# Kernel optimization log

Hardware: AMD Instinct MI355X
Metric: run time of the kernel (lower is better)

The kernel has to match this reference:

```python
import jax, jax.numpy as jnp
import numpy as np

SR = 16000
HOP = 256
MIN_F0 = 50.0
MAX_F0 = 500.0
MIN_PERIOD = SR // 500          # 32
MAX_PERIOD = SR // 50           # 320
FRAME_LEN = HOP * 2             # 512
LAG_END = min(MAX_PERIOD, FRAME_LEN // 2)  # 256 -> lags 32..255 (224 lags)


def setup_inputs() -> dict:
    key = jax.random.key(0)
    waveform = jax.random.normal(key, (64, 1, 163840), dtype=jnp.float32)
    return {"waveform": waveform}


def reference(waveform):
    B, C, T = waveform.shape
    x = waveform[:, 0, :]  # (B, T)
    pad = FRAME_LEN // 2
    xpad = jnp.pad(x, ((0, 0), (pad, pad)), mode='reflect')
    n_frames = (T + 2 * pad - FRAME_LEN) // HOP + 1  # = T//HOP + 1
    # frame extraction (equivalent to unfold(frame_length, hop))
    idx = np.arange(n_frames)[:, None] * HOP + np.arange(FRAME_LEN)[None, :]
    frames = xpad[:, idx]  # (B, F, L)
    # L2-normalize each frame
    norm = jnp.sqrt(jnp.sum(frames * frames, axis=-1, keepdims=True))
    xn = frames / (norm + 1e-8)
    # zero-pad right so xn[t] * xz[t+p] reproduces frame[:L-p] * frame[p:]
    xz = jnp.pad(xn, ((0, 0), (0, 0), (0, FRAME_LEN)))
    lags = jnp.arange(MIN_PERIOD, LAG_END)

    def step(carry, p):
        sl = jax.lax.dynamic_slice_in_dim(xz, p, FRAME_LEN, axis=-1)
        return carry, jnp.sum(xn * sl, axis=-1)  # (B, F)

    _, ac = jax.lax.scan(step, None, lags)  # (P, B, F)
    max_idx = jnp.argmax(ac, axis=0)  # (B, F)
    period = max_idx.astype(jnp.float32) + MIN_PERIOD
    f0 = SR / (period + 1e-8)
    return jnp.clip(f0, MIN_F0, MAX_F0)  # (B, F)
```

## Files before the change

### kernel.cpp

```cpp
#include <hip/hip_runtime.h>


#define SR_F 16000.0f
#define HOP 256
#define FRAME_LEN 512
#define PAD 256
#define T_LEN 163840
#define N_FRAMES 641
#define MIN_PERIOD 32
#define N_LAGS 224
#define WPB 4

typedef _Float16 half8 __attribute__((ext_vector_type(8)));
typedef float floatx4 __attribute__((ext_vector_type(4)));

__device__ __forceinline__ int swz(int q) { return q ^ ((q >> 3) & 7); }

__device__ __forceinline__ unsigned int pkh(float a, float b) {
    unsigned short ha = __builtin_bit_cast(unsigned short, (_Float16)a);
    unsigned short hb = __builtin_bit_cast(unsigned short, (_Float16)b);
    return (unsigned int)ha | ((unsigned int)hb << 16);
}

__device__ __forceinline__ void write_copies(unsigned int* e, unsigned int* o,
                                             unsigned int u10, unsigned int u11,
                                             unsigned int u20, unsigned int u21,
                                             int lane) {
    e[120 + 2*lane] = u10;  e[121 + 2*lane] = u11;
    e[248 + 2*lane] = u20;  e[249 + 2*lane] = u21;
    unsigned int a  = __shfl(u10, (lane + 1) & 63);
    unsigned int bb = __shfl(u20, (lane + 1) & 63);
    unsigned int n1 = (lane == 63) ? bb : a;
    unsigned int n2 = (lane == 63) ? 0u : bb;
    o[120 + 2*lane] = (u10 >> 16) | (u11 << 16);
    o[121 + 2*lane] = (u11 >> 16) | (n1 << 16);
    o[248 + 2*lane] = (u20 >> 16) | (u21 << 16);
    o[249 + 2*lane] = (u21 >> 16) | (n2 << 16);
    if (lane == 0) o[119] = u10 << 16;
}

__global__ __launch_bounds__(256, 4) void f0_kernel(const float* __restrict__ wav,
                                                    float* __restrict__ out) {
    __shared__ unsigned int yw[WPB][1600];

    const int tid  = threadIdx.x;
    const int wv   = tid >> 6;
    const int lane = tid & 63;
    unsigned int* ye  = yw[wv];
    unsigned int* yo  = ye + 400;
    unsigned int* le  = ye + 800;
    unsigned int* loo = ye + 1200;

    const int xcd = blockIdx.x & 7;
    const int idx = blockIdx.x >> 3;
    const int bf  = (xcd * 1282 + idx) * WPB + wv;
    const int b   = bf / N_FRAMES;
    const int f   = bf - b * N_FRAMES;
    const float* __restrict__ x = wav + (size_t)b * T_LEN;
    const int base = f * HOP - PAD;
    const bool fast = (f != 0 && f != N_FRAMES - 1);

    const int qd = lane >> 4;
    const int nn = lane & 15;
    const int par = nn & 1;
    const unsigned int* ybh = par ? yo : ye;
    const unsigned int* ybl = par ? loo : le;
    const int wA0 = 120 + 4*qd - 8*nn;
    const int wB0 = 136 + 4*qd + ((nn - par) >> 1);
    const int seg = lane & 15;
    const bool s0 = (seg & 1), s1 = (seg & 2), s2 = (seg & 4), s3 = (seg & 8);

    float4 c1, c2;
    if (fast) {
        const float4* g4 = (const float4*)(x + base);
        c1 = g4[lane];
        c2 = g4[lane + 64];
    }
    ye[lane] = 0u; yo[lane] = 0u;
    if (lane < 56) { ye[64 + lane] = 0u; yo[64 + lane] = 0u; }
    if (lane < 25) { ye[375 + lane] = 0u; yo[375 + lane] = 0u; }

    float qen = 0.0f;
    if (fast) {
        qen = c1.x*c1.x + c1.y*c1.y + c1.z*c1.z + c1.w*c1.w
            + c2.x*c2.x + c2.y*c2.y + c2.z*c2.z + c2.w*c2.w;
        write_copies(ye, yo, pkh(c1.x, c1.y), pkh(c1.z, c1.w),
                             pkh(c2.x, c2.y), pkh(c2.z, c2.w), lane);
    } else {
        for (int t = lane; t < FRAME_LEN; t += 64) {
            int idxr = base + t;
            if (idxr < 0) idxr = -idxr;
            if (idxr >= T_LEN) idxr = 2 * (T_LEN - 1) - idxr;
            float v = x[idxr];
            qen = __builtin_fmaf(v, v, qen);
            unsigned short h = __builtin_bit_cast(unsigned short, (_Float16)v);
            ((unsigned short*)ye)[240 + t] = h;
            ((unsigned short*)yo)[239 + t] = h;
        }
    }
    __threadfence_block();

    #pragma unroll
    for (int m = 1; m < 64; m <<= 1) qen += __shfl_xor(qen, m);

    floatx4 acc0 = {0.f, 0.f, 0.f, 0.f};
    floatx4 acc1 = {0.f, 0.f, 0.f, 0.f};
    #pragma unroll
    for (int c = 0; c < 16; c += 2) {
        uint4 au0 = *(const uint4*)(ye + (wA0 + 16*c));
        const unsigned int* pb0 = ybh + (wB0 + 16*c);
        uint4 bu0; bu0.x=pb0[0]; bu0.y=pb0[1]; bu0.z=pb0[2]; bu0.w=pb0[3];
        uint4 au1 = *(const uint4*)(ye + (wA0 + 16*(c+1)));
        const unsigned int* pb1 = ybh + (wB0 + 16*(c+1));
        uint4 bu1; bu1.x=pb1[0]; bu1.y=pb1[1]; bu1.z=pb1[2]; bu1.w=pb1[3];
        acc0 = __builtin_amdgcn_mfma_f32_16x16x32_f16(
            __builtin_bit_cast(half8, au0), __builtin_bit_cast(half8, bu0),
            acc0, 0, 0, 0);
        acc1 = __builtin_amdgcn_mfma_f32_16x16x32_f16(
            __builtin_bit_cast(half8, au1), __builtin_bit_cast(half8, bu1),
            acc1, 0, 0, 0);
    }
    floatx4 acc = acc0 + acc1;

    float v1 = acc[0];
    int   i1 = 64*qd + nn;
    float v2 = -__builtin_inff();
    #pragma unroll
    for (int r = 1; r < 4; ++r) {
        float cv = (4*qd + r < 14) ? acc[r] : -__builtin_inff();
        bool take = (cv > v1);
        float lose = take ? v1 : cv;
        if (take) { v1 = cv; i1 = 64*qd + 16*r + nn; }
        v2 = fmaxf(v2, lose);
    }
    #pragma unroll
    for (int m = 1; m < 64; m <<= 1) {
        float ov1 = __shfl_xor(v1, m);
        float ov2 = __shfl_xor(v2, m);
        int   oi1 = __shfl_xor(i1, m);
        bool take = (ov1 > v1) || (ov1 == v1 && oi1 < i1);
        float lose = take ? v1 : ov1;
        if (take) { v1 = ov1; i1 = oi1; }
        v2 = fmaxf(fmaxf(v2, ov2), lose);
    }

    const float E1 = 9.765625e-4f * qen + 0.05f;
    if (v1 - v2 > 2.0f * E1) {
        if (lane == 0) {
            float period = (float)(i1 + MIN_PERIOD);
            float f0 = SR_F / (period + 1e-8f);
            out[bf] = fminf(fmaxf(f0, 50.0f), 500.0f);
        }
        return;
    }

    le[lane] = 0u; loo[lane] = 0u;
    if (lane < 56) { le[64 + lane] = 0u; loo[64 + lane] = 0u; }
    if (lane < 25) { le[375 + lane] = 0u; loo[375 + lane] = 0u; }
    if (fast) {
        float l0 = c1.x - (float)(_Float16)c1.x;
        float l1 = c1.y - (float)(_Float16)c1.y;
        float l2 = c1.z - (float)(_Float16)c1.z;
        float l3 = c1.w - (float)(_Float16)c1.w;
        float l4 = c2.x - (float)(_Float16)c2.x;
        float l5 = c2.y - (float)(_Float16)c2.y;
        float l6 = c2.z - (float)(_Float16)c2.z;
        float l7 = c2.w - (float)(_Float16)c2.w;
        write_copies(le, loo, pkh(l0, l1), pkh(l2, l3),
                              pkh(l4, l5), pkh(l6, l7), lane);
    } else {
        for (int t = lane; t < FRAME_LEN; t += 64) {
            int idxr = base + t;
            if (idxr < 0) idxr = -idxr;
            if (idxr >= T_LEN) idxr = 2 * (T_LEN - 1) - idxr;
            float v = x[idxr];
            float l = v - (float)(_Float16)v;
            unsigned short h = __builtin_bit_cast(unsigned short, (_Float16)l);
            ((unsigned short*)le)[240 + t] = h;
            ((unsigned short*)loo)[239 + t] = h;
        }
    }
    __threadfence_block();

    #pragma unroll
    for (int c = 0; c < 16; ++c) {
        uint4 au = *(const uint4*)(ye + (wA0 + 16*c));
        const unsigned int* pb = ybl + (wB0 + 16*c);
        uint4 bu; bu.x = pb[0]; bu.y = pb[1]; bu.z = pb[2]; bu.w = pb[3];
        acc = __builtin_amdgcn_mfma_f32_16x16x32_f16(
            __builtin_bit_cast(half8, au), __builtin_bit_cast(half8, bu),
            acc, 0, 0, 0);
    }
    #pragma unroll
    for (int c = 0; c < 16; ++c) {
        uint4 au = *(const uint4*)(le + (wA0 + 16*c));
        const unsigned int* pb = ybh + (wB0 + 16*c);
        uint4 bu; bu.x = pb[0]; bu.y = pb[1]; bu.z = pb[2]; bu.w = pb[3];
        acc = __builtin_amdgcn_mfma_f32_16x16x32_f16(
            __builtin_bit_cast(half8, au), __builtin_bit_cast(half8, bu),
            acc, 0, 0, 0);
    }

    v1 = acc[0]; i1 = 64*qd + nn; v2 = -__builtin_inff();
    #pragma unroll
    for (int r = 1; r < 4; ++r) {
        float cv = (4*qd + r < 14) ? acc[r] : -__builtin_inff();
        bool take = (cv > v1);
        float lose = take ? v1 : cv;
        if (take) { v1 = cv; i1 = 64*qd + 16*r + nn; }
        v2 = fmaxf(v2, lose);
    }
    #pragma unroll
    for (int m = 1; m < 64; m <<= 1) {
        float ov1 = __shfl_xor(v1, m);
        float ov2 = __shfl_xor(v2, m);
        int   oi1 = __shfl_xor(i1, m);
        bool take = (ov1 > v1) || (ov1 == v1 && oi1 < i1);
        float lose = take ? v1 : ov1;
        if (take) { v1 = ov1; i1 = oi1; }
        v2 = fmaxf(fmaxf(v2, ov2), lose);
    }

    const float E2 = 1.0e-4f * qen + 0.02f;
    if (v1 - v2 > 2.0f * E2) {
        if (lane == 0) {
            float period = (float)(i1 + MIN_PERIOD);
            float f0 = SR_F / (period + 1e-8f);
            out[bf] = fminf(fmaxf(f0, 50.0f), 500.0f);
        }
        return;
    }

    float* sw = (float*)ye;
    if (fast) {
        const float4* g4 = (const float4*)(x + base);
        ((float4*)sw)[swz(lane)]      = g4[lane];
        ((float4*)sw)[swz(lane + 64)] = g4[lane + 64];
        if (lane < 16) ((float4*)sw)[swz(lane + 128)] = make_float4(0.f,0.f,0.f,0.f);
    } else {
        for (int t = lane; t < FRAME_LEN; t += 64) {
            int idxr = base + t;
            if (idxr < 0) idxr = -idxr;
            if (idxr >= T_LEN) idxr = 2 * (T_LEN - 1) - idxr;
            sw[(swz(t >> 2) << 2) | (t & 3)] = x[idxr];
        }
        int t = FRAME_LEN + lane;
        sw[(swz(t >> 2) << 2) | (t & 3)] = 0.0f;
    }
    __threadfence_block();

    const float4* s4 = (const float4*)sw;
    double dtot[4];
    #pragma unroll
    for (int r = 0; r < 4; ++r) {
        const int g  = (r << 2) + qd;
        const int p0 = MIN_PERIOD + (g << 4);
        double dacc[16];
        #pragma unroll
        for (int j = 0; j < 16; ++j) dacc[j] = 0.0;
        if (g < 14) {
            const int n16 = (FRAME_LEN - p0 + 15) >> 4;
            #pragma unroll
            for (int k = 0; k < 2; ++k) {
                const int ch = seg + (k << 4);
                if (ch < n16) {
                    const int t  = ch << 4;
                    const int qa = t >> 2;
                    const int qw = (t + p0) >> 2;
                    float a[16], w[32];
                    #pragma unroll
                    for (int u = 0; u < 4; ++u) {
                        float4 v = s4[swz(qa + u)];
                        a[4*u+0]=v.x; a[4*u+1]=v.y; a[4*u+2]=v.z; a[4*u+3]=v.w;
                    }
                    #pragma unroll
                    for (int u = 0; u < 8; ++u) {
                        float4 v = s4[swz(qw + u)];
                        w[4*u+0]=v.x; w[4*u+1]=v.y; w[4*u+2]=v.z; w[4*u+3]=v.w;
                    }
                    #pragma unroll
                    for (int j = 0; j < 16; ++j) {
                        #pragma unroll
                        for (int i = 0; i < 16; ++i)
                            dacc[j] = fma((double)a[i], (double)w[i + j], dacc[j]);
                    }
                }
            }
        }
        double u8[8], u4[4], u2[2], dtotal;
        #pragma unroll
        for (int i = 0; i < 8; ++i) {
            double lo = dacc[2*i], hi = dacc[2*i+1];
            double keep = s0 ? hi : lo, send = s0 ? lo : hi;
            u8[i] = keep + __shfl_xor(send, 1);
        }
        #pragma unroll
        for (int i = 0; i < 4; ++i) {
            double lo = u8[2*i], hi = u8[2*i+1];
            double keep = s1 ? hi : lo, send = s1 ? lo : hi;
            u4[i] = keep + __shfl_xor(send, 2);
        }
        #pragma unroll
        for (int i = 0; i < 2; ++i) {
            double lo = u4[2*i], hi = u4[2*i+1];
            double keep = s2 ? hi : lo, send = s2 ? lo : hi;
            u2[i] = keep + __shfl_xor(send, 4);
        }
        {
            double lo = u2[0], hi = u2[1];
            double keep = s3 ? hi : lo, send = s3 ? lo : hi;
            dtotal = keep + __shfl_xor(send, 8);
        }
        dtot[r] = ((r << 6) + lane < N_LAGS) ? dtotal : -__builtin_inf();
    }
    double dv1 = dtot[0];
    int    di1 = lane;
    #pragma unroll
    for (int r = 1; r < 4; ++r) {
        double c = dtot[r];
        if (c > dv1) { dv1 = c; di1 = (r << 6) + lane; }
    }
    #pragma unroll
    for (int m = 1; m < 64; m <<= 1) {
        double o = __shfl_xor(dv1, m);
        int   oi = __shfl_xor(di1, m);
        if (o > dv1 || (o == dv1 && oi < di1)) { dv1 = o; di1 = oi; }
    }
    if (lane == 0) {
        float period = (float)(di1 + MIN_PERIOD);
        float f0 = SR_F / (period + 1e-8f);
        out[bf] = fminf(fmaxf(f0, 50.0f), 500.0f);
    }
}

extern "C" void kernel_launch(void* const* d_in, const int* in_sizes, int n_in,
                              void* d_out, int out_size, void* d_ws, size_t ws_size,
                              hipStream_t stream) {
    const float* wav = (const float*)d_in[0];
    float* out = (float*)d_out;
    const int n_blocks = (64 * N_FRAMES) / WPB;
    f0_kernel<<<n_blocks, 256, 0, stream>>>(wav, out);
}
```

Baseline: 133.1 us.

## Split tiered f0 refinement into separate kernels with compacted work lists

Replaces the single kernel, in which each wave could fall through up to three precision tiers, with three kernels. A cheap fp16 MFMA pass handles every frame and appends ambiguous frames to a global list via atomics. A second kernel does the hi/lo split-precision pass only on the listed frames, and a third does the fp64 exact pass on what remains. Each kernel gets its own LDS footprint and launch bounds, so the common tier runs at higher occupancy and the rare tiers are not stranded in divergent waves. This adds extra launches, global atomics and list traffic, and the later kernels are sized with fixed grids whatever the list length.

```diff
diff --git a/kernel.cpp b/kernel.cpp
--- a/kernel.cpp
+++ b/kernel.cpp
@@ -7,12 +7,30 @@
 #define PAD 256
 #define T_LEN 163840
 #define N_FRAMES 641
+#define TOTAL (64 * N_FRAMES)
 #define MIN_PERIOD 32
 #define N_LAGS 224
-#define WPB 4
+
+#define A_BLOCKS 1536
+#define A_WPB 4
+#define A_WAVES (A_BLOCKS * A_WPB)
+#define A_CHUNK 7
+
+#define B_BLOCKS 512
+#define B_WPB 4
+#define B_WAVES (B_BLOCKS * B_WPB)
+
+#define C_BLOCKS 128
+#define C_WPB 4
+#define C_WAVES (C_BLOCKS * C_WPB)
 
 typedef _Float16 half8 __attribute__((ext_vector_type(8)));
 typedef float floatx4 __attribute__((ext_vector_type(4)));
+
+__device__ unsigned int g_cnt2;
+__device__ unsigned int g_cnt3;
+__device__ unsigned int g_lst2[TOTAL];
+__device__ unsigned int g_lst3[TOTAL];
 
 __device__ __forceinline__ int swz(int q) { return q ^ ((q >> 3) & 7); }
 
@@ -39,70 +57,9 @@
     if (lane == 0) o[119] = u10 << 16;
 }
 
-__global__ __launch_bounds__(256, 4) void f0_kernel(const float* __restrict__ wav,
-                                                    float* __restrict__ out) {
-    __shared__ unsigned int yw[WPB][1600];
-
-    const int tid  = threadIdx.x;
-    const int wv   = tid >> 6;
-    const int lane = tid & 63;
-    unsigned int* ye  = yw[wv];
-    unsigned int* yo  = ye + 400;
-    unsigned int* le  = ye + 800;
-    unsigned int* loo = ye + 1200;
-
-    const int xcd = blockIdx.x & 7;
-    const int idx = blockIdx.x >> 3;
-    const int bf  = (xcd * 1282 + idx) * WPB + wv;
-    const int b   = bf / N_FRAMES;
-    const int f   = bf - b * N_FRAMES;
-    const float* __restrict__ x = wav + (size_t)b * T_LEN;
-    const int base = f * HOP - PAD;
-    const bool fast = (f != 0 && f != N_FRAMES - 1);
-
-    const int qd = lane >> 4;
-    const int nn = lane & 15;
-    const int par = nn & 1;
-    const unsigned int* ybh = par ? yo : ye;
-    const unsigned int* ybl = par ? loo : le;
-    const int wA0 = 120 + 4*qd - 8*nn;
-    const int wB0 = 136 + 4*qd + ((nn - par) >> 1);
-    const int seg = lane & 15;
-    const bool s0 = (seg & 1), s1 = (seg & 2), s2 = (seg & 4), s3 = (seg & 8);
-
-    float4 c1, c2;
-    if (fast) {
-        const float4* g4 = (const float4*)(x + base);
-        c1 = g4[lane];
-        c2 = g4[lane + 64];
-    }
-    ye[lane] = 0u; yo[lane] = 0u;
-    if (lane < 56) { ye[64 + lane] = 0u; yo[64 + lane] = 0u; }
-    if (lane < 25) { ye[375 + lane] = 0u; yo[375 + lane] = 0u; }
-
-    float qen = 0.0f;
-    if (fast) {
-        qen = c1.x*c1.x + c1.y*c1.y + c1.z*c1.z + c1.w*c1.w
-            + c2.x*c2.x + c2.y*c2.y + c2.z*c2.z + c2.w*c2.w;
-        write_copies(ye, yo, pkh(c1.x, c1.y), pkh(c1.z, c1.w),
-                             pkh(c2.x, c2.y), pkh(c2.z, c2.w), lane);
-    } else {
-        for (int t = lane; t < FRAME_LEN; t += 64) {
-            int idxr = base + t;
-            if (idxr < 0) idxr = -idxr;
-            if (idxr >= T_LEN) idxr = 2 * (T_LEN - 1) - idxr;
-            float v = x[idxr];
-            qen = __builtin_fmaf(v, v, qen);
-            unsigned short h = __builtin_bit_cast(unsigned short, (_Float16)v);
-            ((unsigned short*)ye)[240 + t] = h;
-            ((unsigned short*)yo)[239 + t] = h;
-        }
-    }
-    __threadfence_block();
-
-    #pragma unroll
-    for (int m = 1; m < 64; m <<= 1) qen += __shfl_xor(qen, m);
-
+__device__ __forceinline__ floatx4 mfma16_2chain(const unsigned int* ye,
+                                                 const unsigned int* ybh,
+                                                 int wA0, int wB0) {
     floatx4 acc0 = {0.f, 0.f, 0.f, 0.f};
     floatx4 acc1 = {0.f, 0.f, 0.f, 0.f};
     #pragma unroll
@@ -120,11 +77,30 @@
             __builtin_bit_cast(half8, au1), __builtin_bit_cast(half8, bu1),
             acc1, 0, 0, 0);
     }
-    floatx4 acc = acc0 + acc1;
-
-    float v1 = acc[0];
-    int   i1 = 64*qd + nn;
-    float v2 = -__builtin_inff();
+    return acc0 + acc1;
+}
+
+__device__ __forceinline__ floatx4 mfma16_chain(floatx4 acc,
+                                                const unsigned int* pa,
+                                                const unsigned int* pb,
+                                                int wA0, int wB0) {
+    #pragma unroll
+    for (int c = 0; c < 16; ++c) {
+        uint4 au = *(const uint4*)(pa + (wA0 + 16*c));
+        const unsigned int* p = pb + (wB0 + 16*c);
+        uint4 bu; bu.x = p[0]; bu.y = p[1]; bu.z = p[2]; bu.w = p[3];
+        acc = __builtin_amdgcn_mfma_f32_16x16x32_f16(
+            __builtin_bit_cast(half8, au), __builtin_bit_cast(half8, bu),
+            acc, 0, 0, 0);
+    }
+    return acc;
+}
+
+__device__ __forceinline__ void top2(floatx4 acc, int qd, int nn,
+                                     float& v1, int& i1, float& v2) {
+    v1 = acc[0];
+    i1 = 64*qd + nn;
+    v2 = -__builtin_inff();
     #pragma unroll
     for (int r = 1; r < 4; ++r) {
         float cv = (4*qd + r < 14) ? acc[r] : -__builtin_inff();
@@ -143,193 +119,307 @@
         if (take) { v1 = ov1; i1 = oi1; }
         v2 = fmaxf(fmaxf(v2, ov2), lose);
     }
-
-    const float E1 = 9.765625e-4f * qen + 0.05f;
-    if (v1 - v2 > 2.0f * E1) {
+}
+
+__device__ __forceinline__ void emit(float* out, int bf, int i1) {
+    float period = (float)(i1 + MIN_PERIOD);
+    float f0 = SR_F / (period + 1e-8f);
+    out[bf] = fminf(fmaxf(f0, 50.0f), 500.0f);
+}
+
+__global__ void f0_zero() {
+    if (threadIdx.x == 0) { g_cnt2 = 0u; g_cnt3 = 0u; }
+}
+
+__global__ __launch_bounds__(256, 8) void f0_t1(const float* __restrict__ wav,
+                                                float* __restrict__ out) {
+    __shared__ unsigned int yw[A_WPB][800];
+    const int tid  = threadIdx.x;
+    const int wv   = tid >> 6;
+    const int lane = tid & 63;
+    unsigned int* ye = yw[wv];
+    unsigned int* yo = ye + 400;
+
+    ye[lane] = 0u; yo[lane] = 0u;
+    if (lane < 56) { ye[64 + lane] = 0u; yo[64 + lane] = 0u; }
+    if (lane < 25) { ye[375 + lane] = 0u; yo[375 + lane] = 0u; }
+
+    const int qd  = lane >> 4;
+    const int nn  = lane & 15;
+    const int par = nn & 1;
+    const unsigned int* ybh = par ? yo : ye;
+    const int wA0 = 120 + 4*qd - 8*nn;
+    const int wB0 = 136 + 4*qd + ((nn - par) >> 1);
+
+    const int cblk = (blockIdx.x & 7) * (A_BLOCKS / 8) + (blockIdx.x >> 3);
+    const int s    = cblk * A_WPB + wv;
+
+    for (int j = 0; j < A_CHUNK; ++j) {
+        const int bf = s * A_CHUNK + j;
+        if (bf >= TOTAL) break;
+        const int b = bf / N_FRAMES;
+        const int f = bf - b * N_FRAMES;
+        const float* __restrict__ x = wav + (size_t)b * T_LEN;
+        const int base = f * HOP - PAD;
+        const bool fastp = (f != 0) && (f != N_FRAMES - 1);
+
+        __threadfence_block();
+        float qen = 0.0f;
+        if (fastp) {
+            const float4* g4 = (const float4*)(x + base);
+            float4 c1 = g4[lane];
+            float4 c2 = g4[lane + 64];
+            qen = c1.x*c1.x + c1.y*c1.y + c1.z*c1.z + c1.w*c1.w
+                + c2.x*c2.x + c2.y*c2.y + c2.z*c2.z + c2.w*c2.w;
+            write_copies(ye, yo, pkh(c1.x, c1.y), pkh(c1.z, c1.w),
+                                 pkh(c2.x, c2.y), pkh(c2.z, c2.w), lane);
+        } else {
+            for (int t = lane; t < FRAME_LEN; t += 64) {
+                int idxr = base + t;
+                if (idxr < 0) idxr = -idxr;
+                if (idxr >= T_LEN) idxr = 2 * (T_LEN - 1) - idxr;
+                float v = x[idxr];
+                qen = __builtin_fmaf(v, v, qen);
+                unsigned short h = __builtin_bit_cast(unsigned short, (_Float16)v);
+                ((unsigned short*)ye)[240 + t] = h;
+                ((unsigned short*)yo)[239 + t] = h;
+            }
+            if (lane == 0) ((unsigned short*)yo)[751] = 0;
+        }
+        __threadfence_block();
+
+        #pragma unroll
+        for (int m = 1; m < 64; m <<= 1) qen += __shfl_xor(qen, m);
+
+        floatx4 acc = mfma16_2chain(ye, ybh, wA0, wB0);
+
+        float v1, v2; int i1;
+        top2(acc, qd, nn, v1, i1, v2);
+
+        const float E1 = 9.765625e-4f * qen + 0.05f;
         if (lane == 0) {
-            float period = (float)(i1 + MIN_PERIOD);
-            float f0 = SR_F / (period + 1e-8f);
-            out[bf] = fminf(fmaxf(f0, 50.0f), 500.0f);
-        }
-        return;
-    }
-
-    le[lane] = 0u; loo[lane] = 0u;
-    if (lane < 56) { le[64 + lane] = 0u; loo[64 + lane] = 0u; }
-    if (lane < 25) { le[375 + lane] = 0u; loo[375 + lane] = 0u; }
-    if (fast) {
-        float l0 = c1.x - (float)(_Float16)c1.x;
-        float l1 = c1.y - (float)(_Float16)c1.y;
-        float l2 = c1.z - (float)(_Float16)c1.z;
-        float l3 = c1.w - (float)(_Float16)c1.w;
-        float l4 = c2.x - (float)(_Float16)c2.x;
-        float l5 = c2.y - (float)(_Float16)c2.y;
-        float l6 = c2.z - (float)(_Float16)c2.z;
-        float l7 = c2.w - (float)(_Float16)c2.w;
-        write_copies(le, loo, pkh(l0, l1), pkh(l2, l3),
-                              pkh(l4, l5), pkh(l6, l7), lane);
-    } else {
-        for (int t = lane; t < FRAME_LEN; t += 64) {
-            int idxr = base + t;
-            if (idxr < 0) idxr = -idxr;
-            if (idxr >= T_LEN) idxr = 2 * (T_LEN - 1) - idxr;
-            float v = x[idxr];
-            float l = v - (float)(_Float16)v;
-            unsigned short h = __builtin_bit_cast(unsigned short, (_Float16)l);
-            ((unsigned short*)le)[240 + t] = h;
-            ((unsigned short*)loo)[239 + t] = h;
-        }
-    }
-    __threadfence_block();
-
-    #pragma unroll
-    for (int c = 0; c < 16; ++c) {
-        uint4 au = *(const uint4*)(ye + (wA0 + 16*c));
-        const unsigned int* pb = ybl + (wB0 + 16*c);
-        uint4 bu; bu.x = pb[0]; bu.y = pb[1]; bu.z = pb[2]; bu.w = pb[3];
-        acc = __builtin_amdgcn_mfma_f32_16x16x32_f16(
-            __builtin_bit_cast(half8, au), __builtin_bit_cast(half8, bu),
-            acc, 0, 0, 0);
-    }
-    #pragma unroll
-    for (int c = 0; c < 16; ++c) {
-        uint4 au = *(const uint4*)(le + (wA0 + 16*c));
-        const unsigned int* pb = ybh + (wB0 + 16*c);
-        uint4 bu; bu.x = pb[0]; bu.y = pb[1]; bu.z = pb[2]; bu.w = pb[3];
-        acc = __builtin_amdgcn_mfma_f32_16x16x32_f16(
-            __builtin_bit_cast(half8, au), __builtin_bit_cast(half8, bu),
-            acc, 0, 0, 0);
-    }
-
-    v1 = acc[0]; i1 = 64*qd + nn; v2 = -__builtin_inff();
-    #pragma unroll
-    for (int r = 1; r < 4; ++r) {
-        float cv = (4*qd + r < 14) ? acc[r] : -__builtin_inff();
-        bool take = (cv > v1);
-        float lose = take ? v1 : cv;
-        if (take) { v1 = cv; i1 = 64*qd + 16*r + nn; }
-        v2 = fmaxf(v2, lose);
-    }
-    #pragma unroll
-    for (int m = 1; m < 64; m <<= 1) {
-        float ov1 = __shfl_xor(v1, m);
-        float ov2 = __shfl_xor(v2, m);
-        int   oi1 = __shfl_xor(i1, m);
-        bool take = (ov1 > v1) || (ov1 == v1 && oi1 < i1);
-        float lose = take ? v1 : ov1;
-        if (take) { v1 = ov1; i1 = oi1; }
-        v2 = fmaxf(fmaxf(v2, ov2), lose);
-    }
-
-    const float E2 = 1.0e-4f * qen + 0.02f;
-    if (v1 - v2 > 2.0f * E2) {
+            if (v1 - v2 > 2.0f * E1) {
+                emit(out, bf, i1);
+            } else {
+                unsigned int ii = atomicAdd(&g_cnt2, 1u);
+                g_lst2[ii] = (unsigned int)bf;
+            }
+        }
+    }
+}
+
+__global__ __launch_bounds__(256, 3) void f0_t2(const float* __restrict__ wav,
+                                                float* __restrict__ out) {
+    __shared__ unsigned int yw[B_WPB][1600];
+    const int tid  = threadIdx.x;
+    const int wv   = tid >> 6;
+    const int lane = tid & 63;
+    unsigned int* ye  = yw[wv];
+    unsigned int* yo  = ye + 400;
+    unsigned int* le  = ye + 800;
+    unsigned int* loo = ye + 1200;
+
+    ye[lane] = 0u; yo[lane] = 0u; le[lane] = 0u; loo[lane] = 0u;
+    if (lane < 56) { ye[64+lane]=0u; yo[64+lane]=0u; le[64+lane]=0u; loo[64+lane]=0u; }
+    if (lane < 25) { ye[375+lane]=0u; yo[375+lane]=0u; le[375+lane]=0u; loo[375+lane]=0u; }
+
+    const int qd  = lane >> 4;
+    const int nn  = lane & 15;
+    const int par = nn & 1;
+    const unsigned int* ybh = par ? yo : ye;
+    const unsigned int* ybl = par ? loo : le;
+    const int wA0 = 120 + 4*qd - 8*nn;
+    const int wB0 = 136 + 4*qd + ((nn - par) >> 1);
+
+    const unsigned int cnt = g_cnt2;
+    for (unsigned int it = blockIdx.x * B_WPB + wv; it < cnt; it += B_WAVES) {
+        const int bf = (int)g_lst2[it];
+        const int b = bf / N_FRAMES;
+        const int f = bf - b * N_FRAMES;
+        const float* __restrict__ x = wav + (size_t)b * T_LEN;
+        const int base = f * HOP - PAD;
+        const bool fastp = (f != 0) && (f != N_FRAMES - 1);
+
+        __threadfence_block();
+        float qen = 0.0f;
+        if (fastp) {
+            const float4* g4 = (const float4*)(x + base);
+            float4 c1 = g4[lane];
+            float4 c2 = g4[lane + 64];
+            qen = c1.x*c1.x + c1.y*c1.y + c1.z*c1.z + c1.w*c1.w
+                + c2.x*c2.x + c2.y*c2.y + c2.z*c2.z + c2.w*c2.w;
+            write_copies(ye, yo, pkh(c1.x, c1.y), pkh(c1.z, c1.w),
+                                 pkh(c2.x, c2.y), pkh(c2.z, c2.w), lane);
+            float l0 = c1.x - (float)(_Float16)c1.x;
+            float l1 = c1.y - (float)(_Float16)c1.y;
+            float l2 = c1.z - (float)(_Float16)c1.z;
+            float l3 = c1.w - (float)(_Float16)c1.w;
+            float l4 = c2.x - (float)(_Float16)c2.x;
+            float l5 = c2.y - (float)(_Float16)c2.y;
+            float l6 = c2.z - (float)(_Float16)c2.z;
+            float l7 = c2.w - (float)(_Float16)c2.w;
+            write_copies(le, loo, pkh(l0, l1), pkh(l2, l3),
+                                  pkh(l4, l5), pkh(l6, l7), lane);
+        } else {
+            for (int t = lane; t < FRAME_LEN; t += 64) {
+                int idxr = base + t;
+                if (idxr < 0) idxr = -idxr;
+                if (idxr >= T_LEN) idxr = 2 * (T_LEN - 1) - idxr;
+                float v = x[idxr];
+                qen = __builtin_fmaf(v, v, qen);
+                float l = v - (float)(_Float16)v;
+                unsigned short h  = __builtin_bit_cast(unsigned short, (_Float16)v);
+                unsigned short hl = __builtin_bit_cast(unsigned short, (_Float16)l);
+                ((unsigned short*)ye)[240 + t] = h;
+                ((unsigned short*)yo)[239 + t] = h;
+                ((unsigned short*)le)[240 + t] = hl;
+                ((unsigned short*)loo)[239 + t] = hl;
+            }
+            if (lane == 0) {
+                ((unsigned short*)yo)[751]  = 0;
+                ((unsigned short*)loo)[751] = 0;
+            }
+        }
+        __threadfence_block();
+
+        #pragma unroll
+        for (int m = 1; m < 64; m <<= 1) qen += __shfl_xor(qen, m);
+
+        floatx4 acc = mfma16_2chain(ye, ybh, wA0, wB0);
+        acc = mfma16_chain(acc, ye, ybl, wA0, wB0);
+        acc = mfma16_chain(acc, le, ybh, wA0, wB0);
+
+        float v1, v2; int i1;
+        top2(acc, qd, nn, v1, i1, v2);
+
+        const float E2 = 1.0e-4f * qen + 0.02f;
         if (lane == 0) {
-            float period = (float)(i1 + MIN_PERIOD);
-            float f0 = SR_F / (period + 1e-8f);
-            out[bf] = fminf(fmaxf(f0, 50.0f), 500.0f);
-        }
-        return;
-    }
-
-    float* sw = (float*)ye;
-    if (fast) {
-        const float4* g4 = (const float4*)(x + base);
-        ((float4*)sw)[swz(lane)]      = g4[lane];
-        ((float4*)sw)[swz(lane + 64)] = g4[lane + 64];
-        if (lane < 16) ((float4*)sw)[swz(lane + 128)] = make_float4(0.f,0.f,0.f,0.f);
-    } else {
-        for (int t = lane; t < FRAME_LEN; t += 64) {
-            int idxr = base + t;
-            if (idxr < 0) idxr = -idxr;
-            if (idxr >= T_LEN) idxr = 2 * (T_LEN - 1) - idxr;
-            sw[(swz(t >> 2) << 2) | (t & 3)] = x[idxr];
-        }
-        int t = FRAME_LEN + lane;
-        sw[(swz(t >> 2) << 2) | (t & 3)] = 0.0f;
-    }
-    __threadfence_block();
-
-    const float4* s4 = (const float4*)sw;
-    double dtot[4];
-    #pragma unroll
-    for (int r = 0; r < 4; ++r) {
-        const int g  = (r << 2) + qd;
-        const int p0 = MIN_PERIOD + (g << 4);
-        double dacc[16];
+            if (v1 - v2 > 2.0f * E2) {
+                emit(out, bf, i1);
+            } else {
+                unsigned int ii = atomicAdd(&g_cnt3, 1u);
+                g_lst3[ii] = (unsigned int)bf;
+            }
+        }
+    }
+}
+
+__global__ __launch_bounds__(256, 2) void f0_t3(const float* __restrict__ wav,
+                                                float* __restrict__ out) {
+    __shared__ float swb[C_WPB][576];
+    const int tid  = threadIdx.x;
+    const int wv   = tid >> 6;
+    const int lane = tid & 63;
+    float* sw = swb[wv];
+    const int qd  = lane >> 4;
+    const int seg = lane & 15;
+    const bool s0 = (seg & 1), s1 = (seg & 2), s2 = (seg & 4), s3 = (seg & 8);
+
+    const unsigned int cnt = g_cnt3;
+    for (unsigned int it = blockIdx.x * C_WPB + wv; it < cnt; it += C_WAVES) {
+        const int bf = (int)g_lst3[it];
+        const int b = bf / N_FRAMES;
+        const int f = bf - b * N_FRAMES;
+        const float* __restrict__ x = wav + (size_t)b * T_LEN;
+        const int base = f * HOP - PAD;
+        const bool fastp = (f != 0) && (f != N_FRAMES - 1);
+
+        __threadfence_block();
+        if (fastp) {
+            const float4* g4 = (const float4*)(x + base);
+            ((float4*)sw)[swz(lane)]      = g4[lane];
+            ((float4*)sw)[swz(lane + 64)] = g4[lane + 64];
+            if (lane < 16) ((float4*)sw)[swz(lane + 128)] = make_float4(0.f,0.f,0.f,0.f);
+        } else {
+            for (int t = lane; t < FRAME_LEN; t += 64) {
+                int idxr = base + t;
+                if (idxr < 0) idxr = -idxr;
+                if (idxr >= T_LEN) idxr = 2 * (T_LEN - 1) - idxr;
+                sw[(swz(t >> 2) << 2) | (t & 3)] = x[idxr];
+            }
+            int t = FRAME_LEN + lane;
+            sw[(swz(t >> 2) << 2) | (t & 3)] = 0.0f;
+        }
+        __threadfence_block();
+
+        const float4* s4 = (const float4*)sw;
+        double dtot[4];
         #pragma unroll
-        for (int j = 0; j < 16; ++j) dacc[j] = 0.0;
-        if (g < 14) {
-            const int n16 = (FRAME_LEN - p0 + 15) >> 4;
+        for (int r = 0; r < 4; ++r) {
+            const int g  = (r << 2) + qd;
+            const int p0 = MIN_PERIOD + (g << 4);
+            double dacc[16];
             #pragma unroll
-            for (int k = 0; k < 2; ++k) {
-                const int ch = seg + (k << 4);
-                if (ch < n16) {
-                    const int t  = ch << 4;
-                    const int qa = t >> 2;
-                    const int qw = (t + p0) >> 2;
-                    float a[16], w[32];
-                    #pragma unroll
-                    for (int u = 0; u < 4; ++u) {
-                        float4 v = s4[swz(qa + u)];
-                        a[4*u+0]=v.x; a[4*u+1]=v.y; a[4*u+2]=v.z; a[4*u+3]=v.w;
-                    }
-                    #pragma unroll
-                    for (int u = 0; u < 8; ++u) {
-                        float4 v = s4[swz(qw + u)];
-                        w[4*u+0]=v.x; w[4*u+1]=v.y; w[4*u+2]=v.z; w[4*u+3]=v.w;
-                    }
-                    #pragma unroll
-                    for (int j = 0; j < 16; ++j) {
+            for (int j = 0; j < 16; ++j) dacc[j] = 0.0;
+            if (g < 14) {
+                const int n16 = (FRAME_LEN - p0 + 15) >> 4;
+                #pragma unroll
+                for (int k = 0; k < 2; ++k) {
+                    const int ch = seg + (k << 4);
+                    if (ch < n16) {
+                        const int t  = ch << 4;
+                        const int qa = t >> 2;
+                        const int qw = (t + p0) >> 2;
+                        float a[16], w[32];
                         #pragma unroll
-                        for (int i = 0; i < 16; ++i)
-                            dacc[j] = fma((double)a[i], (double)w[i + j], dacc[j]);
+                        for (int u = 0; u < 4; ++u) {
+                            float4 v = s4[swz(qa + u)];
+                            a[4*u+0]=v.x; a[4*u+1]=v.y; a[4*u+2]=v.z; a[4*u+3]=v.w;
+                        }
+                        #pragma unroll
+                        for (int u = 0; u < 8; ++u) {
+                            float4 v = s4[swz(qw + u)];
+                            w[4*u+0]=v.x; w[4*u+1]=v.y; w[4*u+2]=v.z; w[4*u+3]=v.w;
+                        }
+                        #pragma unroll
+                        for (int j = 0; j < 16; ++j) {
+                            #pragma unroll
+                            for (int i = 0; i < 16; ++i)
+                                dacc[j] = fma((double)a[i], (double)w[i + j], dacc[j]);
+                        }
                     }
                 }
             }
-        }
-        double u8[8], u4[4], u2[2], dtotal;
+            double u8[8], u4[4], u2[2], dtotal;
+            #pragma unroll
+            for (int i = 0; i < 8; ++i) {
+                double lo = dacc[2*i], hi = dacc[2*i+1];
+                double keep = s0 ? hi : lo, send = s0 ? lo : hi;
+                u8[i] = keep + __shfl_xor(send, 1);
+            }
+            #pragma unroll
+            for (int i = 0; i < 4; ++i) {
+                double lo = u8[2*i], hi = u8[2*i+1];
+                double keep = s1 ? hi : lo, send = s1 ? lo : hi;
+                u4[i] = keep + __shfl_xor(send, 2);
+            }
+            #pragma unroll
+            for (int i = 0; i < 2; ++i) {
+                double lo = u4[2*i], hi = u4[2*i+1];
+                double keep = s2 ? hi : lo, send = s2 ? lo : hi;
+                u2[i] = keep + __shfl_xor(send, 4);
+            }
+            {
+                double lo = u2[0], hi = u2[1];
+                double keep = s3 ? hi : lo, send = s3 ? lo : hi;
+                dtotal = keep + __shfl_xor(send, 8);
+            }
+            dtot[r] = ((r << 6) + lane < N_LAGS) ? dtotal : -__builtin_inf();
+        }
+        double dv1 = dtot[0];
+        int    di1 = lane;
         #pragma unroll
-        for (int i = 0; i < 8; ++i) {
-            double lo = dacc[2*i], hi = dacc[2*i+1];
-            double keep = s0 ? hi : lo, send = s0 ? lo : hi;
-            u8[i] = keep + __shfl_xor(send, 1);
+        for (int r = 1; r < 4; ++r) {
+            double c = dtot[r];
+            if (c > dv1) { dv1 = c; di1 = (r << 6) + lane; }
         }
         #pragma unroll
-        for (int i = 0; i < 4; ++i) {
-            double lo = u8[2*i], hi = u8[2*i+1];
-            double keep = s1 ? hi : lo, send = s1 ? lo : hi;
-            u4[i] = keep + __shfl_xor(send, 2);
-        }
-        #pragma unroll
-        for (int i = 0; i < 2; ++i) {
-            double lo = u4[2*i], hi = u4[2*i+1];
-            double keep = s2 ? hi : lo, send = s2 ? lo : hi;
-            u2[i] = keep + __shfl_xor(send, 4);
-        }
-        {
-            double lo = u2[0], hi = u2[1];
-            double keep = s3 ? hi : lo, send = s3 ? lo : hi;
-            dtotal = keep + __shfl_xor(send, 8);
-        }
-        dtot[r] = ((r << 6) + lane < N_LAGS) ? dtotal : -__builtin_inf();
-    }
-    double dv1 = dtot[0];
-    int    di1 = lane;
-    #pragma unroll
-    for (int r = 1; r < 4; ++r) {
-        double c = dtot[r];
-        if (c > dv1) { dv1 = c; di1 = (r << 6) + lane; }
-    }
-    #pragma unroll
-    for (int m = 1; m < 64; m <<= 1) {
-        double o = __shfl_xor(dv1, m);
-        int   oi = __shfl_xor(di1, m);
-        if (o > dv1 || (o == dv1 && oi < di1)) { dv1 = o; di1 = oi; }
-    }
-    if (lane == 0) {
-        float period = (float)(di1 + MIN_PERIOD);
-        float f0 = SR_F / (period + 1e-8f);
-        out[bf] = fminf(fmaxf(f0, 50.0f), 500.0f);
+        for (int m = 1; m < 64; m <<= 1) {
+            double o = __shfl_xor(dv1, m);
+            int   oi = __shfl_xor(di1, m);
+            if (o > dv1 || (o == dv1 && oi < di1)) { dv1 = o; di1 = oi; }
+        }
+        if (lane == 0) emit(out, bf, di1);
     }
 }
 
@@ -338,6 +428,8 @@
                               hipStream_t stream) {
     const float* wav = (const float*)d_in[0];
     float* out = (float*)d_out;
-    const int n_blocks = (64 * N_FRAMES) / WPB;
-    f0_kernel<<<n_blocks, 256, 0, stream>>>(wav, out);
-}
+    f0_zero<<<1, 64, 0, stream>>>();
+    f0_t1<<<A_BLOCKS, 256, 0, stream>>>(wav, out);
+    f0_t2<<<B_BLOCKS, 256, 0, stream>>>(wav, out);
+    f0_t3<<<C_BLOCKS, 256, 0, stream>>>(wav, out);
+}
```

After: 177.7 us. +33.6%, slower.

## Use four shifted fp16 copies for aligned B loads, DPP reductions, trim MFMA chunks

Applied to the files above, without the earlier changes.

Stores the fp16 frame in four copies shifted by one half-element each, so B operands can be fetched with two 64-bit LDS loads instead of four scalar loads. The dot-product loops are cut from 16 to 15 K-chunks. The wave sum and top-2 argmax reductions now use DPP for their first four steps instead of ds_bpermute shuffles. This adds extra LDS writes and a larger shared footprint per wave, which may reduce occupancy, and it relies on the dropped chunk contributing nothing to the needed lags.

```diff
diff --git a/kernel.cpp b/kernel.cpp
--- a/kernel.cpp
+++ b/kernel.cpp
@@ -10,6 +10,11 @@
 #define MIN_PERIOD 32
 #define N_LAGS 224
 #define WPB 4
+#define CP 402
+#define L0_OFF 1608
+#define L1_OFF 2008
+#define WAVE_DW 2408
+#define NC 15
 
 typedef _Float16 half8 __attribute__((ext_vector_type(8)));
 typedef float floatx4 __attribute__((ext_vector_type(4)));
@@ -22,34 +27,131 @@
     return (unsigned int)ha | ((unsigned int)hb << 16);
 }
 
-__device__ __forceinline__ void write_copies(unsigned int* e, unsigned int* o,
-                                             unsigned int u10, unsigned int u11,
-                                             unsigned int u20, unsigned int u21,
-                                             int lane) {
-    e[120 + 2*lane] = u10;  e[121 + 2*lane] = u11;
-    e[248 + 2*lane] = u20;  e[249 + 2*lane] = u21;
+#define DPP_XOR1 0xB1
+#define DPP_XOR2 0x4E
+#define DPP_ROR4 0x124
+#define DPP_ROR8 0x128
+
+template <int CTRL> __device__ __forceinline__ int dppi(int x) {
+    return __builtin_amdgcn_update_dpp(0, x, CTRL, 0xF, 0xF, false);
+}
+template <int CTRL> __device__ __forceinline__ float dppf(float x) {
+    return __builtin_bit_cast(float, dppi<CTRL>(__builtin_bit_cast(int, x)));
+}
+
+__device__ __forceinline__ float wave_sum(float x) {
+    x += dppf<DPP_XOR1>(x);
+    x += dppf<DPP_XOR2>(x);
+    x += dppf<DPP_ROR4>(x);
+    x += dppf<DPP_ROR8>(x);
+    x += __shfl_xor(x, 16);
+    x += __shfl_xor(x, 32);
+    return x;
+}
+
+template <int CTRL> __device__ __forceinline__
+void top2_dpp(float& v1, int& i1, float& v2) {
+    float ov1 = dppf<CTRL>(v1);
+    int   oi1 = dppi<CTRL>(i1);
+    float ov2 = dppf<CTRL>(v2);
+    bool take = (ov1 > v1) || (ov1 == v1 && oi1 < i1);
+    float lose = take ? v1 : ov1;
+    if (take) { v1 = ov1; i1 = oi1; }
+    v2 = fmaxf(fmaxf(v2, ov2), lose);
+}
+
+__device__ __forceinline__
+void top2_shfl(float& v1, int& i1, float& v2, int m) {
+    float ov1 = __shfl_xor(v1, m);
+    float ov2 = __shfl_xor(v2, m);
+    int   oi1 = __shfl_xor(i1, m);
+    bool take = (ov1 > v1) || (ov1 == v1 && oi1 < i1);
+    float lose = take ? v1 : ov1;
+    if (take) { v1 = ov1; i1 = oi1; }
+    v2 = fmaxf(fmaxf(v2, ov2), lose);
+}
+
+__device__ __forceinline__
+void top2_full(floatx4 acc, int qd, int nn, float& v1, int& i1, float& v2) {
+    v1 = acc[0];
+    i1 = 64*qd + nn;
+    v2 = -__builtin_inff();
+    #pragma unroll
+    for (int r = 1; r < 4; ++r) {
+        float cv = (4*qd + r < 14) ? acc[r] : -__builtin_inff();
+        bool take = (cv > v1);
+        float lose = take ? v1 : cv;
+        if (take) { v1 = cv; i1 = 64*qd + 16*r + nn; }
+        v2 = fmaxf(v2, lose);
+    }
+    top2_dpp<DPP_XOR1>(v1, i1, v2);
+    top2_dpp<DPP_XOR2>(v1, i1, v2);
+    top2_dpp<DPP_ROR4>(v1, i1, v2);
+    top2_dpp<DPP_ROR8>(v1, i1, v2);
+    top2_shfl(v1, i1, v2, 16);
+    top2_shfl(v1, i1, v2, 32);
+}
+
+__device__ __forceinline__ void write_hi4(unsigned int* c0_, unsigned int* c1_,
+                                          unsigned int* c2_, unsigned int* c3_,
+                                          unsigned int u10, unsigned int u11,
+                                          unsigned int u20, unsigned int u21,
+                                          int lane) {
+    *(unsigned long long*)(c0_ + 120 + 2*lane) =
+        ((unsigned long long)u11 << 32) | u10;
+    *(unsigned long long*)(c0_ + 248 + 2*lane) =
+        ((unsigned long long)u21 << 32) | u20;
     unsigned int a  = __shfl(u10, (lane + 1) & 63);
     unsigned int bb = __shfl(u20, (lane + 1) & 63);
     unsigned int n1 = (lane == 63) ? bb : a;
     unsigned int n2 = (lane == 63) ? 0u : bb;
-    o[120 + 2*lane] = (u10 >> 16) | (u11 << 16);
-    o[121 + 2*lane] = (u11 >> 16) | (n1 << 16);
-    o[248 + 2*lane] = (u20 >> 16) | (u21 << 16);
-    o[249 + 2*lane] = (u21 >> 16) | (n2 << 16);
-    if (lane == 0) o[119] = u10 << 16;
+    unsigned int o10 = (u10 >> 16) | (u11 << 16);
+    unsigned int o11 = (u11 >> 16) | (n1 << 16);
+    unsigned int o20 = (u20 >> 16) | (u21 << 16);
+    unsigned int o21 = (u21 >> 16) | (n2 << 16);
+    *(unsigned long long*)(c1_ + 120 + 2*lane) =
+        ((unsigned long long)o11 << 32) | o10;
+    *(unsigned long long*)(c1_ + 248 + 2*lane) =
+        ((unsigned long long)o21 << 32) | o20;
+    c2_[119 + 2*lane] = u10; c2_[120 + 2*lane] = u11;
+    c2_[247 + 2*lane] = u20; c2_[248 + 2*lane] = u21;
+    c3_[119 + 2*lane] = o10; c3_[120 + 2*lane] = o11;
+    c3_[247 + 2*lane] = o20; c3_[248 + 2*lane] = o21;
+}
+
+__device__ __forceinline__ void write_lo2(unsigned int* l0_, unsigned int* l1_,
+                                          unsigned int u10, unsigned int u11,
+                                          unsigned int u20, unsigned int u21,
+                                          int lane) {
+    *(unsigned long long*)(l0_ + 120 + 2*lane) =
+        ((unsigned long long)u11 << 32) | u10;
+    *(unsigned long long*)(l0_ + 248 + 2*lane) =
+        ((unsigned long long)u21 << 32) | u20;
+    unsigned int a  = __shfl(u10, (lane + 1) & 63);
+    unsigned int bb = __shfl(u20, (lane + 1) & 63);
+    unsigned int n1 = (lane == 63) ? bb : a;
+    unsigned int n2 = (lane == 63) ? 0u : bb;
+    *(unsigned long long*)(l1_ + 120 + 2*lane) =
+        ((unsigned long long)(((u11 >> 16) | (n1 << 16))) << 32) |
+        ((u10 >> 16) | (u11 << 16));
+    *(unsigned long long*)(l1_ + 248 + 2*lane) =
+        ((unsigned long long)(((u21 >> 16) | (n2 << 16))) << 32) |
+        ((u20 >> 16) | (u21 << 16));
 }
 
 __global__ __launch_bounds__(256, 4) void f0_kernel(const float* __restrict__ wav,
                                                     float* __restrict__ out) {
-    __shared__ unsigned int yw[WPB][1600];
+    __shared__ unsigned int yw[WPB][WAVE_DW];
 
     const int tid  = threadIdx.x;
     const int wv   = tid >> 6;
     const int lane = tid & 63;
-    unsigned int* ye  = yw[wv];
-    unsigned int* yo  = ye + 400;
-    unsigned int* le  = ye + 800;
-    unsigned int* loo = ye + 1200;
+    unsigned int* c0p = yw[wv];
+    unsigned int* c1p = c0p + CP;
+    unsigned int* c2p = c0p + 2*CP;
+    unsigned int* c3p = c0p + 3*CP;
+    unsigned int* l0p = c0p + L0_OFF;
+    unsigned int* l1p = c0p + L1_OFF;
 
     const int xcd = blockIdx.x & 7;
     const int idx = blockIdx.x >> 3;
@@ -63,10 +165,9 @@
     const int qd = lane >> 4;
     const int nn = lane & 15;
     const int par = nn & 1;
-    const unsigned int* ybh = par ? yo : ye;
-    const unsigned int* ybl = par ? loo : le;
     const int wA0 = 120 + 4*qd - 8*nn;
-    const int wB0 = 136 + 4*qd + ((nn - par) >> 1);
+    const unsigned int* bhp = c0p + CP*(nn & 3) + 136 + 4*qd + 2*(nn >> 2);
+    const int wB0old = 136 + 4*qd + ((nn - par) >> 1);
     const int seg = lane & 15;
     const bool s0 = (seg & 1), s1 = (seg & 2), s2 = (seg & 4), s3 = (seg & 8);
 
@@ -76,16 +177,19 @@
         c1 = g4[lane];
         c2 = g4[lane + 64];
     }
-    ye[lane] = 0u; yo[lane] = 0u;
-    if (lane < 56) { ye[64 + lane] = 0u; yo[64 + lane] = 0u; }
-    if (lane < 25) { ye[375 + lane] = 0u; yo[375 + lane] = 0u; }
+    for (int d = lane; d < 120; d += 64) { c0p[d] = 0u; l0p[d] = 0u; }
+    if (lane < 28) {
+        int d = 374 + lane;
+        c0p[d] = 0u; c1p[d] = 0u; c2p[d] = 0u; c3p[d] = 0u;
+        l0p[d] = 0u; l1p[d] = 0u;
+    }
 
     float qen = 0.0f;
     if (fast) {
         qen = c1.x*c1.x + c1.y*c1.y + c1.z*c1.z + c1.w*c1.w
             + c2.x*c2.x + c2.y*c2.y + c2.z*c2.z + c2.w*c2.w;
-        write_copies(ye, yo, pkh(c1.x, c1.y), pkh(c1.z, c1.w),
-                             pkh(c2.x, c2.y), pkh(c2.z, c2.w), lane);
+        write_hi4(c0p, c1p, c2p, c3p, pkh(c1.x, c1.y), pkh(c1.z, c1.w),
+                                      pkh(c2.x, c2.y), pkh(c2.z, c2.w), lane);
     } else {
         for (int t = lane; t < FRAME_LEN; t += 64) {
             int idxr = base + t;
@@ -94,55 +198,38 @@
             float v = x[idxr];
             qen = __builtin_fmaf(v, v, qen);
             unsigned short h = __builtin_bit_cast(unsigned short, (_Float16)v);
-            ((unsigned short*)ye)[240 + t] = h;
-            ((unsigned short*)yo)[239 + t] = h;
+            ((unsigned short*)c0p)[240 + t] = h;
+            ((unsigned short*)c1p)[239 + t] = h;
+            ((unsigned short*)c2p)[238 + t] = h;
+            ((unsigned short*)c3p)[237 + t] = h;
         }
     }
     __threadfence_block();
 
-    #pragma unroll
-    for (int m = 1; m < 64; m <<= 1) qen += __shfl_xor(qen, m);
+    qen = wave_sum(qen);
 
     floatx4 acc0 = {0.f, 0.f, 0.f, 0.f};
     floatx4 acc1 = {0.f, 0.f, 0.f, 0.f};
     #pragma unroll
-    for (int c = 0; c < 16; c += 2) {
-        uint4 au0 = *(const uint4*)(ye + (wA0 + 16*c));
-        const unsigned int* pb0 = ybh + (wB0 + 16*c);
-        uint4 bu0; bu0.x=pb0[0]; bu0.y=pb0[1]; bu0.z=pb0[2]; bu0.w=pb0[3];
-        uint4 au1 = *(const uint4*)(ye + (wA0 + 16*(c+1)));
-        const unsigned int* pb1 = ybh + (wB0 + 16*(c+1));
-        uint4 bu1; bu1.x=pb1[0]; bu1.y=pb1[1]; bu1.z=pb1[2]; bu1.w=pb1[3];
-        acc0 = __builtin_amdgcn_mfma_f32_16x16x32_f16(
-            __builtin_bit_cast(half8, au0), __builtin_bit_cast(half8, bu0),
-            acc0, 0, 0, 0);
-        acc1 = __builtin_amdgcn_mfma_f32_16x16x32_f16(
-            __builtin_bit_cast(half8, au1), __builtin_bit_cast(half8, bu1),
-            acc1, 0, 0, 0);
+    for (int c = 0; c < NC; ++c) {
+        uint4 au = *(const uint4*)(c0p + (wA0 + 16*c));
+        unsigned long long bl = *(const unsigned long long*)(bhp + 16*c);
+        unsigned long long br = *(const unsigned long long*)(bhp + 16*c + 2);
+        uint4 bu; bu.x = (unsigned int)bl; bu.y = (unsigned int)(bl >> 32);
+        bu.z = (unsigned int)br; bu.w = (unsigned int)(br >> 32);
+        if (c & 1)
+            acc1 = __builtin_amdgcn_mfma_f32_16x16x32_f16(
+                __builtin_bit_cast(half8, au), __builtin_bit_cast(half8, bu),
+                acc1, 0, 0, 0);
+        else
+            acc0 = __builtin_amdgcn_mfma_f32_16x16x32_f16(
+                __builtin_bit_cast(half8, au), __builtin_bit_cast(half8, bu),
+                acc0, 0, 0, 0);
     }
     floatx4 acc = acc0 + acc1;
 
-    float v1 = acc[0];
-    int   i1 = 64*qd + nn;
-    float v2 = -__builtin_inff();
-    #pragma unroll
-    for (int r = 1; r < 4; ++r) {
-        float cv = (4*qd + r < 14) ? acc[r] : -__builtin_inff();
-        bool take = (cv > v1);
-        float lose = take ? v1 : cv;
-        if (take) { v1 = cv; i1 = 64*qd + 16*r + nn; }
-        v2 = fmaxf(v2, lose);
-    }
-    #pragma unroll
-    for (int m = 1; m < 64; m <<= 1) {
-        float ov1 = __shfl_xor(v1, m);
-        float ov2 = __shfl_xor(v2, m);
-        int   oi1 = __shfl_xor(i1, m);
-        bool take = (ov1 > v1) || (ov1 == v1 && oi1 < i1);
-        float lose = take ? v1 : ov1;
-        if (take) { v1 = ov1; i1 = oi1; }
-        v2 = fmaxf(fmaxf(v2, ov2), lose);
-    }
+    float v1, v2; int i1;
+    top2_full(acc, qd, nn, v1, i1, v2);
 
     const float E1 = 9.765625e-4f * qen + 0.05f;
     if (v1 - v2 > 2.0f * E1) {
@@ -154,9 +241,6 @@
         return;
     }
 
-    le[lane] = 0u; loo[lane] = 0u;
-    if (lane < 56) { le[64 + lane] = 0u; loo[64 + lane] = 0u; }
-    if (lane < 25) { le[375 + lane] = 0u; loo[375 + lane] = 0u; }
     if (fast) {
         float l0 = c1.x - (float)(_Float16)c1.x;
         float l1 = c1.y - (float)(_Float16)c1.y;
@@ -166,8 +250,8 @@
         float l5 = c2.y - (float)(_Float16)c2.y;
         float l6 = c2.z - (float)(_Float16)c2.z;
         float l7 = c2.w - (float)(_Float16)c2.w;
-        write_copies(le, loo, pkh(l0, l1), pkh(l2, l3),
-                              pkh(l4, l5), pkh(l6, l7), lane);
+        write_lo2(l0p, l1p, pkh(l0, l1), pkh(l2, l3),
+                            pkh(l4, l5), pkh(l6, l7), lane);
     } else {
         for (int t = lane; t < FRAME_LEN; t += 64) {
             int idxr = base + t;
@@ -176,50 +260,35 @@
             float v = x[idxr];
             float l = v - (float)(_Float16)v;
             unsigned short h = __builtin_bit_cast(unsigned short, (_Float16)l);
-            ((unsigned short*)le)[240 + t] = h;
-            ((unsigned short*)loo)[239 + t] = h;
+            ((unsigned short*)l0p)[240 + t] = h;
+            ((unsigned short*)l1p)[239 + t] = h;
         }
     }
     __threadfence_block();
 
-    #pragma unroll
-    for (int c = 0; c < 16; ++c) {
-        uint4 au = *(const uint4*)(ye + (wA0 + 16*c));
-        const unsigned int* pb = ybl + (wB0 + 16*c);
-        uint4 bu; bu.x = pb[0]; bu.y = pb[1]; bu.z = pb[2]; bu.w = pb[3];
+    const unsigned int* ybl = par ? l1p : l0p;
+    #pragma unroll
+    for (int c = 0; c < NC; ++c) {
+        uint4 au = *(const uint4*)(c0p + (wA0 + 16*c));
+        const unsigned int* p = ybl + (wB0old + 16*c);
+        uint4 bu; bu.x = p[0]; bu.y = p[1]; bu.z = p[2]; bu.w = p[3];
         acc = __builtin_amdgcn_mfma_f32_16x16x32_f16(
             __builtin_bit_cast(half8, au), __builtin_bit_cast(half8, bu),
             acc, 0, 0, 0);
     }
     #pragma unroll
-    for (int c = 0; c < 16; ++c) {
-        uint4 au = *(const uint4*)(le + (wA0 + 16*c));
-        const unsigned int* pb = ybh + (wB0 + 16*c);
-        uint4 bu; bu.x = pb[0]; bu.y = pb[1]; bu.z = pb[2]; bu.w = pb[3];
+    for (int c = 0; c < NC; ++c) {
+        uint4 au = *(const uint4*)(l0p + (wA0 + 16*c));
+        unsigned long long bl = *(const unsigned long long*)(bhp + 16*c);
+        unsigned long long br = *(const unsigned long long*)(bhp + 16*c + 2);
+        uint4 bu; bu.x = (unsigned int)bl; bu.y = (unsigned int)(bl >> 32);
+        bu.z = (unsigned int)br; bu.w = (unsigned int)(br >> 32);
         acc = __builtin_amdgcn_mfma_f32_16x16x32_f16(
             __builtin_bit_cast(half8, au), __builtin_bit_cast(half8, bu),
             acc, 0, 0, 0);
     }
 
-    v1 = acc[0]; i1 = 64*qd + nn; v2 = -__builtin_inff();
-    #pragma unroll
-    for (int r = 1; r < 4; ++r) {
-        float cv = (4*qd + r < 14) ? acc[r] : -__builtin_inff();
-        bool take = (cv > v1);
-        float lose = take ? v1 : cv;
-        if (take) { v1 = cv; i1 = 64*qd + 16*r + nn; }
-        v2 = fmaxf(v2, lose);
-    }
-    #pragma unroll
-    for (int m = 1; m < 64; m <<= 1) {
-        float ov1 = __shfl_xor(v1, m);
-        float ov2 = __shfl_xor(v2, m);
-        int   oi1 = __shfl_xor(i1, m);
-        bool take = (ov1 > v1) || (ov1 == v1 && oi1 < i1);
-        float lose = take ? v1 : ov1;
-        if (take) { v1 = ov1; i1 = oi1; }
-        v2 = fmaxf(fmaxf(v2, ov2), lose);
-    }
+    top2_full(acc, qd, nn, v1, i1, v2);
 
     const float E2 = 1.0e-4f * qen + 0.02f;
     if (v1 - v2 > 2.0f * E2) {
@@ -231,7 +300,7 @@
         return;
     }
 
-    float* sw = (float*)ye;
+    float* sw = (float*)c0p;
     if (fast) {
         const float4* g4 = (const float4*)(x + base);
         ((float4*)sw)[swz(lane)]      = g4[lane];
```

Result: slower. 135.7 us (+2.0%).
